# Kernel tuning notes

Measured on AMD Instinct MI355X. Metric: run time of the kernel, lower is better.

Reference implementation:

```python
import math
import jax, jax.numpy as jnp
import numpy as np

B, N, F, FE = 16, 24, 128, 128   # crystals, atoms/crystal, atom feat, edge feat
NUM_Z = 100                       # num_atomic_numbers
GAUSS_STOP, BASIS_W = 6.0, 1.0
RADIUS_RATE = 1.0
N_CONV, N_FC, FC_F = 3, 4, 128
REP = 1                           # PBC replication per axis (27 images); exact for our cells
ZDIM = 2 * F + FE


def setup_inputs() -> dict:
    key = jax.random.key(0)
    ks = jax.random.split(key, 12)
    # cubic cells with side length in [8, 10) Angstrom -> rep per axis is exactly 1
    L = 8.0 + 2.0 * jax.random.uniform(ks[0], (B,))
    cell = L[:, None, None] * jnp.eye(3, dtype=jnp.float32)          # [B,3,3]
    frac = jax.random.uniform(ks[1], (B, N, 3))
    pos = jnp.einsum('bnd,bde->bne', frac, cell).reshape(B * N, 3)   # [B*N,3]
    atomic_numbers = jax.random.randint(ks[2], (B * N,), 1, NUM_Z + 1)
    batch = jnp.repeat(jnp.arange(B), N)
    emb = jax.random.normal(ks[3], (NUM_Z, F)) * 0.1                 # embedding table
    s = 1.0 / math.sqrt(ZDIM)
    conv_Wf = jax.random.normal(ks[4], (N_CONV, ZDIM, F)) * s
    conv_bf = jnp.zeros((N_CONV, F))
    conv_Ws = jax.random.normal(ks[5], (N_CONV, ZDIM, F)) * s
    conv_bs = jnp.zeros((N_CONV, F))
    sf = 1.0 / math.sqrt(FC_F)
    fc_W = jax.random.normal(ks[6], (N_FC - 1, FC_F, FC_F)) * sf
    fc_b = jnp.zeros((N_FC - 1, FC_F))
    W_out = jax.random.normal(ks[7], (FC_F, 1)) * sf
    b_out = jnp.zeros((1,))
    return {'pos': pos, 'cell': cell, 'emb': emb,
            'conv_Wf': conv_Wf, 'conv_bf': conv_bf,
            'conv_Ws': conv_Ws, 'conv_bs': conv_bs,
            'fc_W': fc_W, 'fc_b': fc_b, 'W_out': W_out, 'b_out': b_out,
            'atomic_numbers': atomic_numbers, 'batch': batch}


def _spectral_normalize(W, iters=5, eps=1e-12):
    # power iteration; sigma differentiable through W only (u,v detached) as in torch
    u = jnp.ones((W.shape[1],), W.dtype)
    u = u / jnp.linalg.norm(u)
    for _ in range(iters):
        v = W @ u
        v = v / (jnp.linalg.norm(v) + eps)
        u = W.T @ v
        u = u / (jnp.linalg.norm(u) + eps)
    u = jax.lax.stop_gradient(u)
    v = jax.lax.stop_gradient(v)
    sigma = v @ (W @ u)
    return W / sigma


def _forward(pos, cell, emb, conv_Wf, conv_bf, conv_Ws, conv_bs,
             fc_W, fc_b, W_out, b_out, atomic_numbers):
    # ---- graph construction (PBC all-pairs, fixed 27 images, masked) ----
    r = jnp.arange(-REP, REP + 1, dtype=cell.dtype)
    grid = jnp.stack(jnp.meshgrid(r, r, r, indexing='ij'), -1).reshape(-1, 3)  # [27,3]
    pbc = jnp.einsum('cd,bde->bce', grid, cell)                                # [B,27,3]
    posb = pos.reshape(B, N, 3)
    # disp[b,i,j,c] = pos_i - (pos_j + offset_c)
    disp = posb[:, :, None, None, :] - (posb[:, None, :, None, :] + pbc[:, None, None, :, :])
    dsqr = jnp.sum(disp * disp, -1)                                            # [B,N,N,27]
    cross = jnp.cross(cell[:, 1], cell[:, 2])
    vol = jnp.sum(cell[:, 0] * cross, -1)
    radius = RADIUS_RATE * (jnp.abs(vol) / N) ** (1.0 / 3.0)                   # [B]
    rb = radius[:, None, None, None]
    mask = (dsqr <= rb * rb) & (dsqr > 1e-4)
    dist = jnp.sqrt(jnp.maximum(dsqr, 1e-12))
    mf = mask.astype(pos.dtype)
    edge_w = (jnp.cos(dist * math.pi / rb) + 1.0) * mf                         # [B,N,N,27]
    # GaussianSmearing
    goff = jnp.linspace(0.0, GAUSS_STOP, FE)
    coeff = -0.5 / (BASIS_W * (goff[1] - goff[0])) ** 2
    edge_attr = jnp.exp(coeff * (dist[..., None] - goff) ** 2)                 # [B,N,N,27,FE]

    # ---- node features ----
    feat = jnp.tanh(emb[atomic_numbers - 1]).reshape(B, N, F)

    # ---- continuous graph convs (CGCNN-style gated conv, edge_weight scaled) ----
    for l in range(N_CONV):
        Wf, Ws = conv_Wf[l], conv_Ws[l]
        gi = feat @ Wf[:F]; gj = feat @ Wf[F:2 * F]
        ge = jnp.einsum('bijce,ef->bijcf', edge_attr, Wf[2 * F:])
        g = jax.nn.sigmoid(gi[:, :, None, None, :] + gj[:, None, :, None, :] + ge + conv_bf[l])
        si = feat @ Ws[:F]; sj = feat @ Ws[F:2 * F]
        se = jnp.einsum('bijce,ef->bijcf', edge_attr, Ws[2 * F:])
        sc = jax.nn.softplus(si[:, :, None, None, :] + sj[:, None, :, None, :] + se + conv_bs[l])
        msg = g * sc * edge_w[..., None]                                       # [B,N,N,27,F]
        feat = jax.nn.softplus(feat + msg.sum((2, 3)))                         # aggregate at i

    # ---- global mean pool + spectral-norm MLP head ----
    h = feat.mean(1)                                                           # [B,F]
    for l in range(N_FC - 1):
        h = jax.nn.softplus(h @ _spectral_normalize(fc_W[l]) + fc_b[l])
    return h @ W_out + b_out                                                   # [B,1]


def reference(pos, cell, emb, conv_Wf, conv_bf, conv_Ws, conv_bs,
              fc_W, fc_b, W_out, b_out, atomic_numbers, batch):
    return _forward(pos, cell, emb, conv_Wf, conv_bf, conv_Ws, conv_bs,
                    fc_W, fc_b, W_out, b_out, atomic_numbers)
```

## Files before the change

kernel.cpp:

```cpp
#include <hip/hip_runtime.h>
#include <math.h>

#define NB 16
#define NN 24
#define NA 384
#define FF 128
#define CC 27
#define MAXNBR 32
#define MAXE 24
#define NT 20

__device__ float g_sigma[4];
__device__ float g_projA[NA*4*FF];
__device__ float g_projB[NA*4*FF];
__device__ float g_feat [NA*FF];
__device__ __align__(128) int g_ctr[4*NB][32];
__device__ __align__(128) int g_sigdone[32];
__device__ __align__(128) int g_batchdone[32];

__device__ __forceinline__ float softplusf(float x){ return fmaxf(x,0.f) + log1pf(expf(-fabsf(x))); }
__device__ __forceinline__ float sigmoidf(float x){ return 1.f/(1.f+expf(-x)); }
__device__ __forceinline__ void st_agent(float* p, float v){
  __hip_atomic_store(p, v, __ATOMIC_RELAXED, __HIP_MEMORY_SCOPE_AGENT);
}
__device__ __forceinline__ float ld_agent(const float* p){
  return __hip_atomic_load(p, __ATOMIC_RELAXED, __HIP_MEMORY_SCOPE_AGENT);
}

__device__ __forceinline__ void band_dot2(const float* __restrict__ ga, int kmin,
                                          const float* __restrict__ Wf2,
                                          const float* __restrict__ Ws2, int f,
                                          float& ge, float& se)
{
  float g = 0.f, s = 0.f;
  #pragma unroll
  for (int t = 0; t < NT; t++) {
    float a = ga[t];
    int k = kmin + t;
    g += a * Wf2[k*FF+f];
    s += a * Ws2[k*FF+f];
  }
  ge = g; se = s;
}

__device__ __forceinline__ float gemv_q(const float* __restrict__ Wf,
                                        const float* __restrict__ Ws,
                                        const float* s_ft, int q, int f)
{
  const float* W = (q==0) ? Wf : (q==1) ? (Wf + FF*FF) : (q==2) ? Ws : (Ws + FF*FF);
  float s = 0.f;
  #pragma unroll 16
  for (int k = 0; k < FF; k++) s += s_ft[k]*W[k*FF+f];
  return s;
}

__device__ __forceinline__ void publish(int* ctr)
{
  asm volatile("s_waitcnt vmcnt(0)" ::: "memory");
  __syncthreads();
  if (threadIdx.x == 0)
    __hip_atomic_fetch_add(ctr, 1, __ATOMIC_RELAXED, __HIP_MEMORY_SCOPE_AGENT);
}

__device__ __forceinline__ void wait_ge(int* ctr, int target)
{
  if (threadIdx.x == 0) {
    int guard = 0;
    while (__hip_atomic_load(ctr, __ATOMIC_RELAXED, __HIP_MEMORY_SCOPE_AGENT) < target) {
      __builtin_amdgcn_s_sleep(4);
      if (++guard > (1<<18)) break;
    }
  }
  __syncthreads();
}

__global__ void __launch_bounds__(512, 4)
k_fused(const float* __restrict__ pos, const float* __restrict__ cell,
        const float* __restrict__ emb,
        const float* __restrict__ conv_Wf, const float* __restrict__ conv_bf,
        const float* __restrict__ conv_Ws, const float* __restrict__ conv_bs,
        const float* __restrict__ fc_W,  const float* __restrict__ fc_b,
        const float* __restrict__ W_out, const float* __restrict__ b_out,
        const int* __restrict__ z, float* __restrict__ out)
{
  const int tid = threadIdx.x;
  const int q = tid >> 7, f = tid & 127;

  __shared__ float s_ft[FF];
  __shared__ float s_cell[9];
  __shared__ float s_rb;
  __shared__ int   s_cnt;
  __shared__ int   s_nj[MAXNBR];
  __shared__ float s_nd[MAXNBR];
  __shared__ float s_nw[MAXNBR];
  __shared__ float s_ga[MAXE][NT];
  __shared__ int   s_km[MAXE];
  __shared__ float s_ge[MAXE][FF];
  __shared__ float s_se[MAXE][FF];
  __shared__ float s_p[4][FF];
  __shared__ float sm[4][FF];
  __shared__ int   s_last;
  __shared__ float s_hh[FF], s_tmp[FF], s_red[FF];

  if (blockIdx.x < 3) {
    const int m = blockIdx.x;
    const float* W = fc_W + m*FF*FF;
    if (tid < FF) s_hh[tid] = 0.08838834764831845f;
    __syncthreads();
    for (int it = 0; it < 5; it++) {
      { float p = 0.f;
        #pragma unroll
        for (int k = q*32; k < q*32+32; k++) p += W[f*FF+k]*s_hh[k];
        sm[q][f] = p; }
      __syncthreads();
      if (tid < FF) { float s = sm[0][f]+sm[1][f]+sm[2][f]+sm[3][f];
                      s_tmp[f] = s; s_red[f] = s*s; }
      __syncthreads();
      for (int st=64; st>0; st>>=1){ if (tid<st) s_red[tid]+=s_red[tid+st]; __syncthreads(); }
      float nv = sqrtf(s_red[0]) + 1e-12f;
      __syncthreads();
      if (tid < FF) s_tmp[f] /= nv;
      __syncthreads();
      { float p = 0.f;
        #pragma unroll
        for (int r = q*32; r < q*32+32; r++) p += W[r*FF+f]*s_tmp[r];
        sm[q][f] = p; }
      __syncthreads();
      if (tid < FF) { float s = sm[0][f]+sm[1][f]+sm[2][f]+sm[3][f];
                      s_hh[f] = s; s_red[f] = s*s; }
      __syncthreads();
      for (int st=64; st>0; st>>=1){ if (tid<st) s_red[tid]+=s_red[tid+st]; __syncthreads(); }
      float nu = sqrtf(s_red[0]) + 1e-12f;
      __syncthreads();
      if (tid < FF) s_hh[f] /= nu;
      __syncthreads();
    }
    { float p = 0.f;
      #pragma unroll
      for (int k = q*32; k < q*32+32; k++) p += W[f*FF+k]*s_hh[k];
      sm[q][f] = p; }
    __syncthreads();
    if (tid < FF) s_red[f] = s_tmp[f]*(sm[0][f]+sm[1][f]+sm[2][f]+sm[3][f]);
    __syncthreads();
    for (int st=64; st>0; st>>=1){ if (tid<st) s_red[tid]+=s_red[tid+st]; __syncthreads(); }
    if (tid == 0) {
      st_agent(&g_sigma[m], s_red[0]);
      asm volatile("s_waitcnt vmcnt(0)" ::: "memory");
      __hip_atomic_fetch_add(&g_sigdone[0], 1, __ATOMIC_RELAXED, __HIP_MEMORY_SCOPE_AGENT);
    }
    return;
  }

  const int i = (int)blockIdx.x - 3;
  const int b = i / NN;

  if (tid < FF) {
    int zi = z[i]; if (zi < 1) zi = 1; if (zi > 100) zi = 100;
    s_ft[tid] = tanhf(emb[(zi-1)*FF+tid]);
  }
  if (tid >= 256 && tid < 265) s_cell[tid-256] = cell[b*9 + tid - 256];
  if (tid == 500) s_cnt = 0;
  __syncthreads();
  if (tid == 0) {
    const float* c = s_cell;
    float cx = c[4]*c[8] - c[5]*c[7];
    float cy = c[5]*c[6] - c[3]*c[8];
    float cz = c[3]*c[7] - c[4]*c[6];
    float vol = c[0]*cx + c[1]*cy + c[2]*cz;
    s_rb = cbrtf(fabsf(vol)/(float)NN);
  }
  __syncthreads();
  {
    const float rb = s_rb, rb2 = rb*rb;
    const float pix = pos[i*3+0], piy = pos[i*3+1], piz = pos[i*3+2];
    const float PI = 3.14159265358979323846f;
    for (int cand = tid; cand < NN*CC; cand += 512) {
      int j = cand / CC, c = cand - j*CC;
      float gx = (float)(c/9) - 1.0f;
      float gy = (float)((c/3)%3) - 1.0f;
      float gz = (float)(c%3) - 1.0f;
      float ox = gx*s_cell[0] + gy*s_cell[3] + gz*s_cell[6];
      float oy = gx*s_cell[1] + gy*s_cell[4] + gz*s_cell[7];
      float oz = gx*s_cell[2] + gy*s_cell[5] + gz*s_cell[8];
      int jg = b*NN + j;
      float dx = pix - (pos[jg*3+0] + ox);
      float dy = piy - (pos[jg*3+1] + oy);
      float dz = piz - (pos[jg*3+2] + oz);
      float d2 = dx*dx + dy*dy + dz*dz;
      if (d2 <= rb2 && d2 > 1e-4f) {
        float dist = sqrtf(fmaxf(d2, 1e-4f));
        float w = cosf(dist*PI/rb) + 1.0f;
        int slot = atomicAdd(&s_cnt, 1);
        if (slot < MAXNBR) { s_nj[slot] = jg; s_nd[slot] = dist; s_nw[slot] = w; }
      }
    }
  }
  __syncthreads();
  const int n0 = (s_cnt > MAXNBR) ? MAXNBR : s_cnt;
  const int n  = (n0 > MAXE) ? MAXE : n0;

  for (int idx = tid; idx < n*NT; idx += 512) {
    int e = idx / NT, t = idx - e*NT;
    float dist = s_nd[e];
    const float step  = 6.0f/127.0f;
    const float coeff = -0.5f/(step*step);
    int kmin = (int)ceilf(dist/step - 9.0f);
    kmin = kmin < 0 ? 0 : (kmin > 108 ? 108 : kmin);
    if (t == 0) s_km[e] = kmin;
    int k = kmin + t;
    float dd = dist - step*(float)k;
    s_ga[e][t] = expf(coeff*dd*dd);
  }
  __syncthreads();

  { float s0 = gemv_q(conv_Wf, conv_Ws, s_ft, q, f);
    s_p[q][f] = s0;
    st_agent(&g_projA[(i*4+q)*FF+f], s0); }
  publish(&g_ctr[0*NB+b][0]);

  for (int l = 0; l < 3; ++l) {
    const float* projSrc = (l==1) ? g_projB : g_projA;
    const float* Wf2 = conv_Wf + l*3*FF*FF + 2*FF*FF;
    const float* Ws2 = conv_Ws + l*3*FF*FF + 2*FF*FF;
    for (int idx = tid; idx < n*FF; idx += 512) {
      int e = idx >> 7, ff = idx & 127;
      float ge, se;
      band_dot2(&s_ga[e][0], s_km[e], Wf2, Ws2, ff, ge, se);
      s_ge[e][ff] = ge; s_se[e][ff] = se;
    }
    __syncthreads();
    wait_ge(&g_ctr[l*NB+b][0], NN);
    {
      const float gi = s_p[0][f], si = s_p[2][f];
      const float bff = conv_bf[l*FF+f], bsf = conv_bs[l*FF+f];
      float msg = 0.f;
      for (int e = q; e < n; e += 4) {
        int   jg = s_nj[e];
        float w  = s_nw[e];
        float gj = ld_agent(&projSrc[(jg*4+1)*FF+f]);
        float sj = ld_agent(&projSrc[(jg*4+3)*FF+f]);
        msg += sigmoidf(gi + gj + s_ge[e][f] + bff)
             * softplusf(si + sj + s_se[e][f] + bsf) * w;
      }
      sm[q][f] = msg;
    }
    __syncthreads();
    if (tid < FF) {
      s_ft[tid] = softplusf(s_ft[tid] + sm[0][tid] + sm[1][tid]
                                      + sm[2][tid] + sm[3][tid]);
    }
    __syncthreads();
    if (l < 2) {
      const float* WfN = conv_Wf + (l+1)*3*FF*FF;
      const float* WsN = conv_Ws + (l+1)*3*FF*FF;
      float* projDst = (l==0) ? g_projB : g_projA;
      float s1 = gemv_q(WfN, WsN, s_ft, q, f);
      s_p[q][f] = s1;
      st_agent(&projDst[(i*4+q)*FF+f], s1);
      publish(&g_ctr[(l+1)*NB+b][0]);
    }
  }

  if (tid < FF) st_agent(&g_feat[i*FF+tid], s_ft[tid]);
  asm volatile("s_waitcnt vmcnt(0)" ::: "memory");
  __syncthreads();
  if (tid == 0)
    s_last = __hip_atomic_fetch_add(&g_ctr[3*NB+b][0], 1, __ATOMIC_RELAXED,
                                    __HIP_MEMORY_SCOPE_AGENT);
  __syncthreads();
  if (s_last != NN-1) return;

  if (tid == 0) {
    int guard = 0;
    while (__hip_atomic_load(&g_sigdone[0], __ATOMIC_RELAXED, __HIP_MEMORY_SCOPE_AGENT) < 3) {
      __builtin_amdgcn_s_sleep(4);
      if (++guard > (1<<18)) break;
    }
  }
  __syncthreads();
  if (tid < FF) {
    float s0 = 0.f;
    for (int a = 0; a < NN; a++) s0 += ld_agent(&g_feat[(b*NN+a)*FF+tid]);
    s_hh[tid] = s0/(float)NN;
  }
  __syncthreads();
  for (int l = 0; l < 3; l++) {
    { float p = 0.f;
      #pragma unroll
      for (int k = q*32; k < q*32+32; k++) p += s_hh[k]*fc_W[l*FF*FF + k*FF + f];
      sm[q][f] = p; }
    __syncthreads();
    if (tid < FF) {
      float s = sm[0][tid]+sm[1][tid]+sm[2][tid]+sm[3][tid];
      s_tmp[tid] = softplusf(s/ld_agent(&g_sigma[l]) + fc_b[l*FF+tid]);
    }
    __syncthreads();
    if (tid < FF) s_hh[tid] = s_tmp[tid];
    __syncthreads();
  }
  if (tid < FF) s_red[tid] = s_hh[tid]*W_out[tid];
  __syncthreads();
  if (tid < 64) {
    float t = s_red[tid] + s_red[tid+64];
    #pragma unroll
    for (int off = 32; off > 0; off >>= 1) t += __shfl_xor(t, off);
    if (tid == 0) {
      out[b] = t + b_out[0];
      __hip_atomic_store(&g_ctr[0*NB+b][0], 0, __ATOMIC_RELAXED, __HIP_MEMORY_SCOPE_AGENT);
      __hip_atomic_store(&g_ctr[1*NB+b][0], 0, __ATOMIC_RELAXED, __HIP_MEMORY_SCOPE_AGENT);
      __hip_atomic_store(&g_ctr[2*NB+b][0], 0, __ATOMIC_RELAXED, __HIP_MEMORY_SCOPE_AGENT);
      __hip_atomic_store(&g_ctr[3*NB+b][0], 0, __ATOMIC_RELAXED, __HIP_MEMORY_SCOPE_AGENT);
      int d = __hip_atomic_fetch_add(&g_batchdone[0], 1, __ATOMIC_RELAXED,
                                     __HIP_MEMORY_SCOPE_AGENT);
      if (d == NB-1) {
        __hip_atomic_store(&g_batchdone[0], 0, __ATOMIC_RELAXED, __HIP_MEMORY_SCOPE_AGENT);
        __hip_atomic_store(&g_sigdone[0],   0, __ATOMIC_RELAXED, __HIP_MEMORY_SCOPE_AGENT);
      }
    }
  }
}

extern "C" void kernel_launch(void* const* d_in, const int* in_sizes, int n_in,
                              void* d_out, int out_size, void* d_ws, size_t ws_size,
                              hipStream_t stream) {
  const float* pos     = (const float*)d_in[0];
  const float* cell    = (const float*)d_in[1];
  const float* emb     = (const float*)d_in[2];
  const float* conv_Wf = (const float*)d_in[3];
  const float* conv_bf = (const float*)d_in[4];
  const float* conv_Ws = (const float*)d_in[5];
  const float* conv_bs = (const float*)d_in[6];
  const float* fc_W    = (const float*)d_in[7];
  const float* fc_b    = (const float*)d_in[8];
  const float* W_out   = (const float*)d_in[9];
  const float* b_out   = (const float*)d_in[10];
  const int*   z       = (const int*)d_in[11];

  k_fused<<<NA+3, 512, 0, stream>>>(pos, cell, emb, conv_Wf, conv_bf,
                                    conv_Ws, conv_bs, fc_W, fc_b,
                                    W_out, b_out, z, (float*)d_out);
}
```

Baseline: 135.8 us.

## Replace per-crystal counters with per-atom epoch flags and batch neighbor loads

Replaces the per-crystal atomic counters, which made every atom wait for all 24 atoms of its crystal, with a per-atom epoch flag. Each block now waits only on the neighbors it actually uses, checked in parallel by one wavefront with __all. The designated first atom of each crystal waits for all of its atoms' flags before running the pooled MLP head, then resets the flags. The neighbor projection loads are also hoisted into a fixed 6-entry unrolled batch so their global-memory latency overlaps. The price is more flag polling traffic and a fixed assumption of at most 24 edges per atom.

```diff
diff --git a/kernel.cpp b/kernel.cpp
--- a/kernel.cpp
+++ b/kernel.cpp
@@ -14,7 +14,7 @@
 __device__ float g_projA[NA*4*FF];
 __device__ float g_projB[NA*4*FF];
 __device__ float g_feat [NA*FF];
-__device__ __align__(128) int g_ctr[4*NB][32];
+__device__ __align__(128) int g_flag[NA][32];
 __device__ __align__(128) int g_sigdone[32];
 __device__ __align__(128) int g_batchdone[32];
 
@@ -24,6 +24,12 @@
   __hip_atomic_store(p, v, __ATOMIC_RELAXED, __HIP_MEMORY_SCOPE_AGENT);
 }
 __device__ __forceinline__ float ld_agent(const float* p){
+  return __hip_atomic_load(p, __ATOMIC_RELAXED, __HIP_MEMORY_SCOPE_AGENT);
+}
+__device__ __forceinline__ void st_agent_i(int* p, int v){
+  __hip_atomic_store(p, v, __ATOMIC_RELAXED, __HIP_MEMORY_SCOPE_AGENT);
+}
+__device__ __forceinline__ int ld_agent_i(const int* p){
   return __hip_atomic_load(p, __ATOMIC_RELAXED, __HIP_MEMORY_SCOPE_AGENT);
 }
 
@@ -54,19 +60,22 @@
   return s;
 }
 
-__device__ __forceinline__ void publish(int* ctr)
+__device__ __forceinline__ void flag_set(int i, int v)
 {
   asm volatile("s_waitcnt vmcnt(0)" ::: "memory");
   __syncthreads();
-  if (threadIdx.x == 0)
-    __hip_atomic_fetch_add(ctr, 1, __ATOMIC_RELAXED, __HIP_MEMORY_SCOPE_AGENT);
-}
-
-__device__ __forceinline__ void wait_ge(int* ctr, int target)
-{
-  if (threadIdx.x == 0) {
+  if (threadIdx.x == 0) st_agent_i(&g_flag[i][0], v);
+}
+
+__device__ __forceinline__ void wait_nbrs(int n, const int* s_nj, int target)
+{
+  if (threadIdx.x < 64) {
+    int jg = (threadIdx.x < n) ? s_nj[threadIdx.x] : -1;
+    bool sat = (jg < 0);
     int guard = 0;
-    while (__hip_atomic_load(ctr, __ATOMIC_RELAXED, __HIP_MEMORY_SCOPE_AGENT) < target) {
+    for (;;) {
+      if (!sat) sat = (ld_agent_i(&g_flag[jg][0]) >= target);
+      if (__all(sat)) break;
       __builtin_amdgcn_s_sleep(4);
       if (++guard > (1<<18)) break;
     }
@@ -99,7 +108,6 @@
   __shared__ float s_se[MAXE][FF];
   __shared__ float s_p[4][FF];
   __shared__ float sm[4][FF];
-  __shared__ int   s_last;
   __shared__ float s_hh[FF], s_tmp[FF], s_red[FF];
 
   if (blockIdx.x < 3) {
@@ -216,7 +224,7 @@
   { float s0 = gemv_q(conv_Wf, conv_Ws, s_ft, q, f);
     s_p[q][f] = s0;
     st_agent(&g_projA[(i*4+q)*FF+f], s0); }
-  publish(&g_ctr[0*NB+b][0]);
+  flag_set(i, 1);
 
   for (int l = 0; l < 3; ++l) {
     const float* projSrc = (l==1) ? g_projB : g_projA;
@@ -229,18 +237,25 @@
       s_ge[e][ff] = ge; s_se[e][ff] = se;
     }
     __syncthreads();
-    wait_ge(&g_ctr[l*NB+b][0], NN);
+    wait_nbrs(n, s_nj, l+1);
     {
       const float gi = s_p[0][f], si = s_p[2][f];
       const float bff = conv_bf[l*FF+f], bsf = conv_bs[l*FF+f];
+      float gjv[6], sjv[6];
+      #pragma unroll
+      for (int t = 0; t < 6; ++t) {
+        int e = q + 4*t;
+        int jg = (e < n) ? s_nj[e] : 0;
+        gjv[t] = ld_agent(&projSrc[(jg*4+1)*FF+f]);
+        sjv[t] = ld_agent(&projSrc[(jg*4+3)*FF+f]);
+      }
       float msg = 0.f;
-      for (int e = q; e < n; e += 4) {
-        int   jg = s_nj[e];
-        float w  = s_nw[e];
-        float gj = ld_agent(&projSrc[(jg*4+1)*FF+f]);
-        float sj = ld_agent(&projSrc[(jg*4+3)*FF+f]);
-        msg += sigmoidf(gi + gj + s_ge[e][f] + bff)
-             * softplusf(si + sj + s_se[e][f] + bsf) * w;
+      #pragma unroll
+      for (int t = 0; t < 6; ++t) {
+        int e = q + 4*t;
+        if (e < n)
+          msg += sigmoidf(gi + gjv[t] + s_ge[e][f] + bff)
+               * softplusf(si + sjv[t] + s_se[e][f] + bsf) * s_nw[e];
       }
       sm[q][f] = msg;
     }
@@ -257,19 +272,27 @@
       float s1 = gemv_q(WfN, WsN, s_ft, q, f);
       s_p[q][f] = s1;
       st_agent(&projDst[(i*4+q)*FF+f], s1);
-      publish(&g_ctr[(l+1)*NB+b][0]);
+      flag_set(i, l+2);
     }
   }
 
   if (tid < FF) st_agent(&g_feat[i*FF+tid], s_ft[tid]);
-  asm volatile("s_waitcnt vmcnt(0)" ::: "memory");
-  __syncthreads();
-  if (tid == 0)
-    s_last = __hip_atomic_fetch_add(&g_ctr[3*NB+b][0], 1, __ATOMIC_RELAXED,
-                                    __HIP_MEMORY_SCOPE_AGENT);
-  __syncthreads();
-  if (s_last != NN-1) return;
-
+  flag_set(i, 4);
+  if (i != b*NN) return;
+
+  if (tid < 64) {
+    int jg = (tid < NN) ? (b*NN + tid) : -1;
+    bool sat = (jg < 0);
+    int guard = 0;
+    for (;;) {
+      if (!sat) sat = (ld_agent_i(&g_flag[jg][0]) >= 4);
+      if (__all(sat)) break;
+      __builtin_amdgcn_s_sleep(4);
+      if (++guard > (1<<18)) break;
+    }
+  }
+  __syncthreads();
+  if (tid < NN) st_agent_i(&g_flag[b*NN+tid][0], 0);
   if (tid == 0) {
     int guard = 0;
     while (__hip_atomic_load(&g_sigdone[0], __ATOMIC_RELAXED, __HIP_MEMORY_SCOPE_AGENT) < 3) {
@@ -306,10 +329,6 @@
     for (int off = 32; off > 0; off >>= 1) t += __shfl_xor(t, off);
     if (tid == 0) {
       out[b] = t + b_out[0];
-      __hip_atomic_store(&g_ctr[0*NB+b][0], 0, __ATOMIC_RELAXED, __HIP_MEMORY_SCOPE_AGENT);
-      __hip_atomic_store(&g_ctr[1*NB+b][0], 0, __ATOMIC_RELAXED, __HIP_MEMORY_SCOPE_AGENT);
-      __hip_atomic_store(&g_ctr[2*NB+b][0], 0, __ATOMIC_RELAXED, __HIP_MEMORY_SCOPE_AGENT);
-      __hip_atomic_store(&g_ctr[3*NB+b][0], 0, __ATOMIC_RELAXED, __HIP_MEMORY_SCOPE_AGENT);
       int d = __hip_atomic_fetch_add(&g_batchdone[0], 1, __ATOMIC_RELAXED,
                                      __HIP_MEMORY_SCOPE_AGENT);
       if (d == NB-1) {
```

Result: faster. 127.6 us (-6.0%).
